# Kernel optimization log

Measured on AMD Instinct MI355X. Metric: run time of the kernel, lower is better.

Reference implementation:

```python
import jax, jax.numpy as jnp
import numpy as np

B, N, D, L = 32, 1000, 256, 3


def setup_inputs() -> dict:
    key = jax.random.key(0)
    k1, k2, k3, k4 = jax.random.split(key, 4)
    x = jax.random.normal(k1, (B, N, D), dtype=jnp.float32)
    node_feature = jax.random.normal(k2, (B, N, D), dtype=jnp.float32)
    # GCNConv weights (PyG Linear, glorot) and biases, stacked over layers
    scale = jnp.sqrt(6.0 / (D + D)).astype(jnp.float32)
    Ws = jax.random.uniform(k3, (L, D, D), minval=-1.0, maxval=1.0, dtype=jnp.float32) * scale
    bs = jnp.zeros((L, D), dtype=jnp.float32)
    return {"x": x, "node_feature": node_feature, "Ws": Ws, "bs": bs}


def _gcn_norm_adj(n):
    # self_loop=False -> adjacency is all-ones (diagonal included), so
    # add_remaining_self_loops is a no-op; deg = n for every node.
    adj = jnp.ones((n, n), dtype=jnp.float32)
    deg = adj.sum(axis=1)
    dinv = jax.lax.rsqrt(deg)
    return dinv[:, None] * adj * dinv[None, :]  # == ones/n


def reference(x, node_feature, Ws, bs):
    # x is unused by the math (only its size is inspected in the original).
    A_norm = _gcn_norm_adj(node_feature.shape[1])
    h = node_feature
    for l in range(L):
        h = jnp.einsum('bnd,de->bne', h, Ws[l])          # linear transform
        h = jnp.einsum('mn,bnd->bmd', A_norm, h) + bs[l]  # normalized aggregation + bias
        if l < L - 1:
            h = jax.nn.relu(h)  # dropout is identity in eval mode
    update_node_feature = h + node_feature  # residual (unconditional in source)
    return (update_node_feature, node_feature)
```

## Files before the change

### kernel.cpp

```cpp
#include <hip/hip_runtime.h>

#define BB 32
#define NN 1000
#define DD 256
#define SS 50
#define RPS 20
#define ELEMS (BB * NN * DD)

__global__ __launch_bounds__(256) void k_colsum_copy(const float4* __restrict__ nf4,
                                                     float4* __restrict__ out1_4,
                                                     float* __restrict__ partials) {
    const int s = blockIdx.x, b = blockIdx.y, t = threadIdx.x;
    const int r4 = t >> 6, c = t & 63;
    float4 acc = make_float4(0.f, 0.f, 0.f, 0.f);
#pragma unroll
    for (int i = 0; i < RPS / 4; i++) {
        const int n = s * RPS + i * 4 + r4;
        const int idx = (b * NN + n) * (DD / 4) + c;
        float4 v = nf4[idx];
        out1_4[idx] = v;
        acc.x += v.x; acc.y += v.y; acc.z += v.z; acc.w += v.w;
    }
    __shared__ float red[1024];
    ((float4*)red)[r4 * 64 + c] = acc;
    __syncthreads();
    const float sum = red[t] + red[256 + t] + red[512 + t] + red[768 + t];
    partials[(b * SS + s) * DD + t] = sum;
}

__global__ __launch_bounds__(1024) void k_mlp(const float* __restrict__ partials,
                                              const float* __restrict__ Ws,
                                              const float* __restrict__ bsv,
                                              float* __restrict__ hrow) {
    const int b = blockIdx.x, t = threadIdx.x;
    const int d = t & (DD - 1), kq = t >> 8;
    __shared__ float h[DD];
    __shared__ float red[1024];

    float acc = 0.f;
    for (int s = kq; s < SS; s += 4)
        acc += partials[(b * SS + s) * DD + d];
    red[t] = acc;
    __syncthreads();
    if (kq == 0)
        h[d] = (red[d] + red[DD + d] + red[2 * DD + d] + red[3 * DD + d]) * (1.0f / (float)NN);
    __syncthreads();

    for (int l = 0; l < 3; l++) {
        const float* __restrict__ W = Ws + l * DD * DD;
        float a = 0.f;
#pragma unroll 16
        for (int kk = 0; kk < 64; kk++) {
            const int k = kq * 64 + kk;
            a += h[k] * W[k * DD + d];
        }
        __syncthreads();
        red[t] = a;
        __syncthreads();
        if (kq == 0) {
            float o = red[d] + red[DD + d] + red[2 * DD + d] + red[3 * DD + d]
                      + bsv[l * DD + d];
            if (l < 2) o = fmaxf(o, 0.f);
            if (l == 2) hrow[b * DD + d] = o;
            else        h[d] = o;
        }
        __syncthreads();
    }
}

__global__ __launch_bounds__(256) void k_out0(const float4* __restrict__ nf4,
                                              const float* __restrict__ hrow,
                                              float4* __restrict__ out0_4) {
    const int i = blockIdx.x * 256 + threadIdx.x;
    const int e = i * 4;
    const int b = e / (NN * DD);
    const int d0 = e & (DD - 1);
    float4 v = nf4[i];
    float4 hv = *(const float4*)(hrow + b * DD + d0);
    out0_4[i] = make_float4(v.x + hv.x, v.y + hv.y, v.z + hv.z, v.w + hv.w);
}

extern "C" void kernel_launch(void* const* d_in, const int* in_sizes, int n_in,
                              void* d_out, int out_size, void* d_ws, size_t ws_size,
                              hipStream_t stream) {
    const float* nf  = (const float*)d_in[1];
    const float* Ws  = (const float*)d_in[2];
    const float* bsv = (const float*)d_in[3];
    float* out = (float*)d_out;

    float* partials = (float*)d_ws;
    float* hrow     = partials + BB * SS * DD;

    k_colsum_copy<<<dim3(SS, BB), 256, 0, stream>>>((const float4*)nf,
                                                    (float4*)(out + ELEMS), partials);
    k_mlp<<<BB, 1024, 0, stream>>>(partials, Ws, bsv, hrow);
    k_out0<<<(ELEMS / 4) / 256, 256, 0, stream>>>((const float4*)nf, hrow, (float4*)out);
}
```

Baseline: 150.1 us.

## Fuse colsum, MLP and residual into one cooperative kernel keeping input in registers

New measurement: 252.0 us. 1.68x slower.

```diff
diff --git a/kernel.cpp b/kernel.cpp
--- a/kernel.cpp
+++ b/kernel.cpp
@@ -1,98 +1,114 @@
 #include <hip/hip_runtime.h>
+#include <hip/hip_cooperative_groups.h>
+
+namespace cg = cooperative_groups;
 
 #define BB 32
 #define NN 1000
 #define DD 256
-#define SS 50
-#define RPS 20
+#define SP 8
+#define CHUNK_ROWS (NN / SP)
+#define CHUNK_F4 (CHUNK_ROWS * DD / 4)
 #define ELEMS (BB * NN * DD)
 
-__global__ __launch_bounds__(256) void k_colsum_copy(const float4* __restrict__ nf4,
-                                                     float4* __restrict__ out1_4,
-                                                     float* __restrict__ partials) {
-    const int s = blockIdx.x, b = blockIdx.y, t = threadIdx.x;
-    const int r4 = t >> 6, c = t & 63;
+__global__ __launch_bounds__(1024) void k_fused(const float4* __restrict__ nf4,
+                                                const float* __restrict__ Ws,
+                                                const float* __restrict__ bsv,
+                                                float4* __restrict__ out0_4,
+                                                float4* __restrict__ out1_4,
+                                                float* __restrict__ partials,
+                                                float* __restrict__ hrow) {
+    const int bid = blockIdx.x, t = threadIdx.x;
+    const int b = bid >> 3, s = bid & (SP - 1);
+    const int base = (b * NN + s * CHUNK_ROWS) * (DD / 4);
+    const int c = t & 63;
+    __shared__ float redA[4096];
+    __shared__ float red[1024];
+    __shared__ float h[DD];
+
+    float4 vv[8];
     float4 acc = make_float4(0.f, 0.f, 0.f, 0.f);
 #pragma unroll
-    for (int i = 0; i < RPS / 4; i++) {
-        const int n = s * RPS + i * 4 + r4;
-        const int idx = (b * NN + n) * (DD / 4) + c;
-        float4 v = nf4[idx];
-        out1_4[idx] = v;
-        acc.x += v.x; acc.y += v.y; acc.z += v.z; acc.w += v.w;
+    for (int k = 0; k < 8; k++) {
+        const int f4o = t + k * 1024;
+        if (f4o < CHUNK_F4) {
+            float4 v = nf4[base + f4o];
+            vv[k] = v;
+            out1_4[base + f4o] = v;
+            acc.x += v.x; acc.y += v.y; acc.z += v.z; acc.w += v.w;
+        }
     }
-    __shared__ float red[1024];
-    ((float4*)red)[r4 * 64 + c] = acc;
+    ((float4*)redA)[(t >> 6) * 64 + c] = acc;
     __syncthreads();
-    const float sum = red[t] + red[256 + t] + red[512 + t] + red[768 + t];
-    partials[(b * SS + s) * DD + t] = sum;
-}
+    if (t < DD) {
+        float sum = 0.f;
+#pragma unroll
+        for (int r = 0; r < 16; r++) sum += redA[r * DD + t];
+        partials[(b * SP + s) * DD + t] = sum;
+    }
 
-__global__ __launch_bounds__(1024) void k_mlp(const float* __restrict__ partials,
-                                              const float* __restrict__ Ws,
-                                              const float* __restrict__ bsv,
-                                              float* __restrict__ hrow) {
-    const int b = blockIdx.x, t = threadIdx.x;
-    const int d = t & (DD - 1), kq = t >> 8;
-    __shared__ float h[DD];
-    __shared__ float red[1024];
+    cg::this_grid().sync();
 
-    float acc = 0.f;
-    for (int s = kq; s < SS; s += 4)
-        acc += partials[(b * SS + s) * DD + d];
-    red[t] = acc;
-    __syncthreads();
-    if (kq == 0)
-        h[d] = (red[d] + red[DD + d] + red[2 * DD + d] + red[3 * DD + d]) * (1.0f / (float)NN);
-    __syncthreads();
+    if (bid < BB) {
+        const int d = t & (DD - 1), kq = t >> 8;
+        float pa = partials[(bid * SP + kq) * DD + d]
+                 + partials[(bid * SP + kq + 4) * DD + d];
+        red[t] = pa;
+        __syncthreads();
+        if (kq == 0)
+            h[d] = (red[d] + red[DD + d] + red[2 * DD + d] + red[3 * DD + d])
+                   * (1.0f / (float)NN);
+        __syncthreads();
+        for (int l = 0; l < 3; l++) {
+            const float* __restrict__ W = Ws + l * DD * DD;
+            float a = 0.f;
+#pragma unroll
+            for (int kk = 0; kk < 64; kk++) {
+                const int k = kq * 64 + kk;
+                a += h[k] * W[k * DD + d];
+            }
+            __syncthreads();
+            red[t] = a;
+            __syncthreads();
+            if (kq == 0) {
+                float o = red[d] + red[DD + d] + red[2 * DD + d] + red[3 * DD + d]
+                          + bsv[l * DD + d];
+                if (l < 2) o = fmaxf(o, 0.f);
+                if (l == 2) hrow[bid * DD + d] = o;
+                else        h[d] = o;
+            }
+            __syncthreads();
+        }
+    }
 
-    for (int l = 0; l < 3; l++) {
-        const float* __restrict__ W = Ws + l * DD * DD;
-        float a = 0.f;
-#pragma unroll 16
-        for (int kk = 0; kk < 64; kk++) {
-            const int k = kq * 64 + kk;
-            a += h[k] * W[k * DD + d];
+    cg::this_grid().sync();
+
+    const float4 hv = *(const float4*)(hrow + b * DD + c * 4);
+#pragma unroll
+    for (int k = 0; k < 8; k++) {
+        const int f4o = t + k * 1024;
+        if (f4o < CHUNK_F4) {
+            float4 v = vv[k];
+            out0_4[base + f4o] = make_float4(v.x + hv.x, v.y + hv.y,
+                                             v.z + hv.z, v.w + hv.w);
         }
-        __syncthreads();
-        red[t] = a;
-        __syncthreads();
-        if (kq == 0) {
-            float o = red[d] + red[DD + d] + red[2 * DD + d] + red[3 * DD + d]
-                      + bsv[l * DD + d];
-            if (l < 2) o = fmaxf(o, 0.f);
-            if (l == 2) hrow[b * DD + d] = o;
-            else        h[d] = o;
-        }
-        __syncthreads();
     }
-}
-
-__global__ __launch_bounds__(256) void k_out0(const float4* __restrict__ nf4,
-                                              const float* __restrict__ hrow,
-                                              float4* __restrict__ out0_4) {
-    const int i = blockIdx.x * 256 + threadIdx.x;
-    const int e = i * 4;
-    const int b = e / (NN * DD);
-    const int d0 = e & (DD - 1);
-    float4 v = nf4[i];
-    float4 hv = *(const float4*)(hrow + b * DD + d0);
-    out0_4[i] = make_float4(v.x + hv.x, v.y + hv.y, v.z + hv.z, v.w + hv.w);
 }
 
 extern "C" void kernel_launch(void* const* d_in, const int* in_sizes, int n_in,
                               void* d_out, int out_size, void* d_ws, size_t ws_size,
                               hipStream_t stream) {
-    const float* nf  = (const float*)d_in[1];
-    const float* Ws  = (const float*)d_in[2];
-    const float* bsv = (const float*)d_in[3];
-    float* out = (float*)d_out;
+    const float4* nf4 = (const float4*)d_in[1];
+    const float* Ws   = (const float*)d_in[2];
+    const float* bsv  = (const float*)d_in[3];
+    float4* out0 = (float4*)d_out;
+    float4* out1 = (float4*)((float*)d_out + ELEMS);
 
     float* partials = (float*)d_ws;
-    float* hrow     = partials + BB * SS * DD;
+    float* hrow     = partials + BB * SP * DD;
 
-    k_colsum_copy<<<dim3(SS, BB), 256, 0, stream>>>((const float4*)nf,
-                                                    (float4*)(out + ELEMS), partials);
-    k_mlp<<<BB, 1024, 0, stream>>>(partials, Ws, bsv, hrow);
-    k_out0<<<(ELEMS / 4) / 256, 256, 0, stream>>>((const float4*)nf, hrow, (float4*)out);
+    void* args[] = {(void*)&nf4, (void*)&Ws, (void*)&bsv, (void*)&out0,
+                    (void*)&out1, (void*)&partials, (void*)&hrow};
+    hipLaunchCooperativeKernel(k_fused, dim3(BB * SP), dim3(1024),
+                               args, 0u, stream);
 }
```

## Prefetch weights into L2 during column-sum pass and slim the MLP kernel

Applied to the files above, without the earlier changes.

New measurement: 134.3 us. 10.5% less time.

```diff
diff --git a/kernel.cpp b/kernel.cpp
--- a/kernel.cpp
+++ b/kernel.cpp
@@ -3,96 +3,111 @@
 #define BB 32
 #define NN 1000
 #define DD 256
-#define SS 50
-#define RPS 20
+#define SS 25
+#define RPS 40
 #define ELEMS (BB * NN * DD)
+#define WF4 (3 * DD * DD / 4)
 
-__global__ __launch_bounds__(256) void k_colsum_copy(const float4* __restrict__ nf4,
-                                                     float4* __restrict__ out1_4,
-                                                     float* __restrict__ partials) {
+typedef float f4 __attribute__((ext_vector_type(4)));
+
+__global__ __launch_bounds__(256) void k_sumcopy(const f4* __restrict__ nf4,
+                                                 f4* __restrict__ out1_4,
+                                                 float* __restrict__ partials,
+                                                 const f4* __restrict__ W4) {
     const int s = blockIdx.x, b = blockIdx.y, t = threadIdx.x;
     const int r4 = t >> 6, c = t & 63;
-    float4 acc = make_float4(0.f, 0.f, 0.f, 0.f);
+    f4 acc = (f4)(0.f);
 #pragma unroll
     for (int i = 0; i < RPS / 4; i++) {
         const int n = s * RPS + i * 4 + r4;
         const int idx = (b * NN + n) * (DD / 4) + c;
-        float4 v = nf4[idx];
+        f4 v = nf4[idx];
         out1_4[idx] = v;
-        acc.x += v.x; acc.y += v.y; acc.z += v.z; acc.w += v.w;
+        acc += v;
+    }
+    {
+        const int bid = b * SS + s;
+#pragma unroll
+        for (int i = 0; i < 2; i++) {
+            const int idx = (bid * 512 + i * 256 + t) % WF4;
+            f4 w = W4[idx];
+            asm volatile("" :: "v"(w.x), "v"(w.y), "v"(w.z), "v"(w.w));
+        }
     }
     __shared__ float red[1024];
-    ((float4*)red)[r4 * 64 + c] = acc;
+    ((f4*)red)[r4 * 64 + c] = acc;
     __syncthreads();
-    const float sum = red[t] + red[256 + t] + red[512 + t] + red[768 + t];
-    partials[(b * SS + s) * DD + t] = sum;
+    partials[(b * SS + s) * DD + t] =
+        red[t] + red[256 + t] + red[512 + t] + red[768 + t];
 }
 
-__global__ __launch_bounds__(1024) void k_mlp(const float* __restrict__ partials,
-                                              const float* __restrict__ Ws,
-                                              const float* __restrict__ bsv,
-                                              float* __restrict__ hrow) {
+__global__ __launch_bounds__(256) void k_mlp(const float* __restrict__ partials,
+                                             const float* __restrict__ Ws,
+                                             const float* __restrict__ bsv,
+                                             float* __restrict__ hrow) {
     const int b = blockIdx.x, t = threadIdx.x;
-    const int d = t & (DD - 1), kq = t >> 8;
-    __shared__ float h[DD];
-    __shared__ float red[1024];
+    __shared__ float h[2][DD];
 
-    float acc = 0.f;
-    for (int s = kq; s < SS; s += 4)
-        acc += partials[(b * SS + s) * DD + d];
-    red[t] = acc;
-    __syncthreads();
-    if (kq == 0)
-        h[d] = (red[d] + red[DD + d] + red[2 * DD + d] + red[3 * DD + d]) * (1.0f / (float)NN);
+    float a0 = 0.f, a1 = 0.f, a2 = 0.f, a3 = 0.f;
+#pragma unroll
+    for (int sp = 0; sp < 24; sp += 4) {
+        a0 += partials[(b * SS + sp + 0) * DD + t];
+        a1 += partials[(b * SS + sp + 1) * DD + t];
+        a2 += partials[(b * SS + sp + 2) * DD + t];
+        a3 += partials[(b * SS + sp + 3) * DD + t];
+    }
+    a0 += partials[(b * SS + 24) * DD + t];
+    h[0][t] = ((a0 + a1) + (a2 + a3)) * (1.0f / (float)NN);
     __syncthreads();
 
+    int cur = 0;
     for (int l = 0; l < 3; l++) {
         const float* __restrict__ W = Ws + l * DD * DD;
-        float a = 0.f;
-#pragma unroll 16
-        for (int kk = 0; kk < 64; kk++) {
-            const int k = kq * 64 + kk;
-            a += h[k] * W[k * DD + d];
+        float c0 = 0.f, c1 = 0.f, c2 = 0.f, c3 = 0.f;
+#pragma unroll 8
+        for (int k4 = 0; k4 < DD / 4; k4++) {
+            const float* Wk = W + (k4 * 4) * DD + t;
+            c0 = fmaf(h[cur][k4 * 4 + 0], Wk[0 * DD], c0);
+            c1 = fmaf(h[cur][k4 * 4 + 1], Wk[1 * DD], c1);
+            c2 = fmaf(h[cur][k4 * 4 + 2], Wk[2 * DD], c2);
+            c3 = fmaf(h[cur][k4 * 4 + 3], Wk[3 * DD], c3);
         }
-        __syncthreads();
-        red[t] = a;
-        __syncthreads();
-        if (kq == 0) {
-            float o = red[d] + red[DD + d] + red[2 * DD + d] + red[3 * DD + d]
-                      + bsv[l * DD + d];
-            if (l < 2) o = fmaxf(o, 0.f);
-            if (l == 2) hrow[b * DD + d] = o;
-            else        h[d] = o;
+        float a = ((c0 + c1) + (c2 + c3)) + bsv[l * DD + t];
+        if (l < 2) {
+            h[cur ^ 1][t] = fmaxf(a, 0.f);
+            cur ^= 1;
+            __syncthreads();
+        } else {
+            hrow[b * DD + t] = a;
         }
-        __syncthreads();
     }
 }
 
-__global__ __launch_bounds__(256) void k_out0(const float4* __restrict__ nf4,
+__global__ __launch_bounds__(256) void k_out0(const f4* __restrict__ nf4,
                                               const float* __restrict__ hrow,
-                                              float4* __restrict__ out0_4) {
+                                              f4* __restrict__ out0_4) {
     const int i = blockIdx.x * 256 + threadIdx.x;
     const int e = i * 4;
     const int b = e / (NN * DD);
     const int d0 = e & (DD - 1);
-    float4 v = nf4[i];
-    float4 hv = *(const float4*)(hrow + b * DD + d0);
-    out0_4[i] = make_float4(v.x + hv.x, v.y + hv.y, v.z + hv.z, v.w + hv.w);
+    f4 v = nf4[i];
+    const f4 hv = *(const f4*)(hrow + b * DD + d0);
+    out0_4[i] = v + hv;
 }
 
 extern "C" void kernel_launch(void* const* d_in, const int* in_sizes, int n_in,
                               void* d_out, int out_size, void* d_ws, size_t ws_size,
                               hipStream_t stream) {
-    const float* nf  = (const float*)d_in[1];
+    const f4* nf4    = (const f4*)d_in[1];
     const float* Ws  = (const float*)d_in[2];
     const float* bsv = (const float*)d_in[3];
-    float* out = (float*)d_out;
+    f4* out0 = (f4*)d_out;
+    f4* out1 = (f4*)((float*)d_out + ELEMS);
 
     float* partials = (float*)d_ws;
-    float* hrow     = partials + BB * SS * DD;
+    float* hrow     = partials + SS * BB * DD;
 
-    k_colsum_copy<<<dim3(SS, BB), 256, 0, stream>>>((const float4*)nf,
-                                                    (float4*)(out + ELEMS), partials);
-    k_mlp<<<BB, 1024, 0, stream>>>(partials, Ws, bsv, hrow);
-    k_out0<<<(ELEMS / 4) / 256, 256, 0, stream>>>((const float4*)nf, hrow, (float4*)out);
+    k_sumcopy<<<dim3(SS, BB), 256, 0, stream>>>(nf4, out1, partials, (const f4*)Ws);
+    k_mlp<<<BB, 256, 0, stream>>>(partials, Ws, bsv, hrow);
+    k_out0<<<(ELEMS / 4) / 256, 256, 0, stream>>>(nf4, hrow, out0);
 }
```
